# Performance work log

Hardware: AMD Instinct MI355X
Metric: run time of the kernel (lower is better)

## Reference

```python
import jax, jax.numpy as jnp
import numpy as np

B, L, C = 32, 8192, 64
LEVELS = 3  # detail kernels 3,5,9 with pads 1,2,4


def _conv1d(x, w, b, pad):
    # x: [B, C, L], w: [O, I, K] (torch Conv1d layout), b: [O]
    y = jax.lax.conv_general_dilated(
        x, w, window_strides=(1,), padding=[(pad, pad)],
        dimension_numbers=('NCH', 'OIH', 'NCH'))
    return y + b[None, :, None]


def _block(xc, w1, b1, w2, b2, pad):
    # Conv1d(k) -> ReLU -> Conv1d(k=1)
    h = jax.nn.relu(_conv1d(xc, w1, b1, pad))
    return _conv1d(h, w2, b2, 0)


def setup_inputs() -> dict:
    key = jax.random.key(0)
    ks = jax.random.split(key, 20)
    s = 0.05  # keep activations stable
    inp = {
        'x': jax.random.normal(ks[0], (B, L, C), jnp.float32),
        'rec_weights': jnp.ones((LEVELS + 1,), jnp.float32) / (LEVELS + 1),
        'trend_w1': jax.random.normal(ks[1], (C, C, 3), jnp.float32) * s,
        'trend_b1': jnp.zeros((C,), jnp.float32),
        'trend_w2': jax.random.normal(ks[2], (C, C, 1), jnp.float32) * s,
        'trend_b2': jnp.zeros((C,), jnp.float32),
    }
    kernels = [3, 5, 9]
    for i, k in enumerate(kernels, start=1):
        inp[f'd{i}_w1'] = jax.random.normal(ks[2 + 2 * i], (C, C, k), jnp.float32) * s
        inp[f'd{i}_b1'] = jnp.zeros((C,), jnp.float32)
        inp[f'd{i}_w2'] = jax.random.normal(ks[3 + 2 * i], (C, C, 1), jnp.float32) * s
        inp[f'd{i}_b2'] = jnp.zeros((C,), jnp.float32)
    return inp


def reference(x, rec_weights,
              trend_w1, trend_b1, trend_w2, trend_b2,
              d1_w1, d1_b1, d1_w2, d1_b2,
              d2_w1, d2_b1, d2_w2, d2_b2,
              d3_w1, d3_b1, d3_w2, d3_b2):
    # component_fusion forward: x [B, L, C] -> [B, L, C]
    xc = jnp.transpose(x, (0, 2, 1))  # [B, C, L]
    trend = _block(xc, trend_w1, trend_b1, trend_w2, trend_b2, 1)
    d1 = _block(xc, d1_w1, d1_b1, d1_w2, d1_b2, 1)   # k=3, pad=1
    d2 = _block(xc, d2_w1, d2_b1, d2_w2, d2_b2, 2)   # k=5, pad=2
    d3 = _block(xc, d3_w1, d3_b1, d3_w2, d3_b2, 4)   # k=9, pad=4
    w = jax.nn.softmax(rec_weights)
    fused = w[0] * trend + w[1] * d1 + w[2] * d2 + w[3] * d3
    return jnp.transpose(fused, (0, 2, 1))
```

## Files before the change

### kernel.cpp

```cpp
#include <hip/hip_runtime.h>


constexpr int Bn = 32, Ln = 8192;
constexpr int NT = 256;
constexpr int HALO = 4;
constexpr int XROWS = NT + 2 * HALO;
constexpr int RS = 72;
constexpr int NSLICE = 24;

using bf16x8 = __attribute__((ext_vector_type(8))) __bf16;
using f32x4  = __attribute__((ext_vector_type(4))) float;
using u16x8  = __attribute__((ext_vector_type(8))) unsigned short;
using u16x4  = __attribute__((ext_vector_type(4))) unsigned short;
using s16x4  = __attribute__((ext_vector_type(4))) short;

struct Ptrs {
    const float* x;
    const float* rw;
    const float* w1[4];
    const float* b1[4];
    const float* w2[4];
    const float* b2[4];
};

__device__ __forceinline__ unsigned short f2bf(float f) {
    __bf16 h = (__bf16)f;
    return __builtin_bit_cast(unsigned short, h);
}

#if defined(__has_builtin)
#  if __has_builtin(__builtin_amdgcn_mfma_f32_16x16x16bf16_1k)
#    define HAVE_MFMA16 1
#  endif
#endif

__device__ __forceinline__ void mfma16(f32x4& c, u16x4 a, u16x4 b) {
#ifdef HAVE_MFMA16
    c = __builtin_amdgcn_mfma_f32_16x16x16bf16_1k(
            __builtin_bit_cast(s16x4, a), __builtin_bit_cast(s16x4, b), c, 0, 0, 0);
#else
    asm("v_mfma_f32_16x16x16_bf16 %0, %1, %2, %0" : "+v"(c) : "v"(a), "v"(b));
#endif
}

__device__ __forceinline__ void stage_slice(const unsigned short* __restrict__ frag,
                                            unsigned short* wbuf, int s, int tid) {
    const unsigned short* g = frag + (size_t)s * 4096 + tid * 8;
    unsigned short* l = wbuf + (s & 1) * 4096 + tid * 8;
    __builtin_amdgcn_global_load_lds(
        (const __attribute__((address_space(1))) unsigned int*)g,
        (__attribute__((address_space(3))) unsigned int*)l, 16, 0, 0);
    __builtin_amdgcn_global_load_lds(
        (const __attribute__((address_space(1))) unsigned int*)(g + 2048),
        (__attribute__((address_space(3))) unsigned int*)(l + 2048), 16, 0, 0);
}

__device__ __forceinline__ void wait_bar_vm2() {
    asm volatile("s_waitcnt vmcnt(2)" ::: "memory");
    __builtin_amdgcn_sched_barrier(0);
    __builtin_amdgcn_s_barrier();
    __builtin_amdgcn_sched_barrier(0);
}
__device__ __forceinline__ void wait_bar_vm0() {
    asm volatile("s_waitcnt vmcnt(0)" ::: "memory");
    __builtin_amdgcn_sched_barrier(0);
    __builtin_amdgcn_s_barrier();
    __builtin_amdgcn_sched_barrier(0);
}
__device__ __forceinline__ void end_bar() {
    __builtin_amdgcn_sched_barrier(0);
    __builtin_amdgcn_s_barrier();
    __builtin_amdgcn_sched_barrier(0);
}

__global__ void prep_kernel(Ptrs p, unsigned short* __restrict__ frag, float* __restrict__ hdr) {
    int tid = threadIdx.x;
    float v0 = p.rw[0], v1 = p.rw[1], v2 = p.rw[2], v3 = p.rw[3];
    float m = fmaxf(fmaxf(v0, v1), fmaxf(v2, v3));
    float e0 = expf(v0 - m), e1 = expf(v1 - m), e2 = expf(v2 - m), e3 = expf(v3 - m);
    float s = e0 + e1 + e2 + e3;
    float w[4] = {e0 / s, e1 / s, e2 / s, e3 / s};

    if (blockIdx.x == 0) {
        if (tid < 4) hdr[tid] = w[tid];
        if (tid < 64) {
            float fb = 0.f;
            #pragma unroll
            for (int i = 0; i < 4; i++) fb += w[i] * p.b2[i][tid];
            hdr[4 + tid] = fb;
        }
    }

    const int kk[4] = {3, 3, 5, 9};
    const int sbase[4] = {0, 4, 8, 14};

    for (int idx = blockIdx.x * blockDim.x + tid; idx < NSLICE * 4096; idx += gridDim.x * blockDim.x) {
        int sl = idx >> 12;
        int e = idx & 4095;
        int br = 3;
        #pragma unroll
        for (int i = 2; i >= 0; i--) if (sl < sbase[i + 1]) br = i;
        int local = sl - sbase[br];
        unsigned short val;
        if (local < kk[br]) {
            int blk = e >> 9;
            int ks = blk >> 2, mt = blk & 3;
            int sub = e & 511;
            int lane = sub >> 3, j = sub & 7;
            int co = mt * 16 + (lane & 15);
            int ci = ks * 32 + (lane >> 4) * 8 + j;
            val = f2bf(p.w1[br][(co * 64 + ci) * kk[br] + local]);
        } else {
            int fi = e >> 8;
            int kb = fi >> 2, mt = fi & 3;
            int sub = e & 255;
            int lane = sub >> 2, j = sub & 3;
            int co = mt * 16 + (lane & 15);
            int ci = kb * 16 + (lane >> 4) * 4 + j;
            val = f2bf(w[br] * p.w2[br][co * 64 + ci]);
        }
        frag[idx] = val;
    }
}

template <int KK, int PP, int S0>
__device__ __forceinline__ void do_branch(const unsigned short* __restrict__ frag,
                                          unsigned short* wbuf,
                                          const float* b1l,
                                          const unsigned short* xs,
                                          int tid, int lane, int wl0,
                                          f32x4 (&fused)[4][4]) {
    int col = lane & 15, kg = lane >> 4;

    f32x4 acc[4][4];
    #pragma unroll
    for (int mt = 0; mt < 4; mt++)
        #pragma unroll
        for (int nt = 0; nt < 4; nt++)
            acc[mt][nt] = f32x4{0.f, 0.f, 0.f, 0.f};

    #pragma unroll
    for (int dk = 0; dk < KK; dk++) {
        stage_slice(frag, wbuf, S0 + dk + 1, tid);
        wait_bar_vm2();
        const unsigned short* wb = wbuf + ((S0 + dk) & 1) * 4096;
        #pragma unroll
        for (int ks = 0; ks < 2; ks++) {
            bf16x8 bfr[4];
            #pragma unroll
            for (int nt = 0; nt < 4; nt++) {
                int row = wl0 + nt * 16 + col + (HALO - PP) + dk;
                bfr[nt] = __builtin_bit_cast(bf16x8, *(const u16x8*)&xs[row * RS + ks * 32 + kg * 8]);
            }
            #pragma unroll
            for (int mt = 0; mt < 4; mt++) {
                bf16x8 afr = __builtin_bit_cast(bf16x8,
                    *(const u16x8*)(wb + (ks * 4 + mt) * 512 + lane * 8));
                #pragma unroll
                for (int nt = 0; nt < 4; nt++)
                    acc[mt][nt] = __builtin_amdgcn_mfma_f32_16x16x32_bf16(afr, bfr[nt], acc[mt][nt], 0, 0, 0);
            }
        }
        end_bar();
    }

    constexpr int SF2 = S0 + KK;
    constexpr bool HN = (SF2 + 1 < NSLICE);
    if constexpr (HN) stage_slice(frag, wbuf, SF2 + 1, tid);

    f32x4 bv[4];
    #pragma unroll
    for (int mt = 0; mt < 4; mt++) bv[mt] = *(const f32x4*)&b1l[mt * 16 + kg * 4];

    if constexpr (HN) wait_bar_vm2(); else wait_bar_vm0();
    const unsigned short* wb2 = wbuf + (SF2 & 1) * 4096;

    #pragma unroll
    for (int kb = 0; kb < 4; kb++) {
        u16x4 hb[4];
        #pragma unroll
        for (int nt = 0; nt < 4; nt++) {
            u16x4 h;
            #pragma unroll
            for (int r = 0; r < 4; r++) h[r] = f2bf(fmaxf(acc[kb][nt][r] + bv[kb][r], 0.f));
            hb[nt] = h;
        }
        #pragma unroll
        for (int mt = 0; mt < 4; mt++) {
            u16x4 afr = *(const u16x4*)(wb2 + (kb * 4 + mt) * 256 + lane * 4);
            #pragma unroll
            for (int nt = 0; nt < 4; nt++)
                mfma16(fused[mt][nt], afr, hb[nt]);
        }
    }
    if constexpr (HN) end_bar();
}

__global__ __launch_bounds__(256, 2) void wavelet_main(Ptrs p,
                                                       const unsigned short* __restrict__ frag,
                                                       const float* __restrict__ hdr,
                                                       float* __restrict__ out) {
    __shared__ unsigned short xs[XROWS * RS];
    __shared__ unsigned short wbuf[2 * 4096];
    __shared__ float b1l[4 * 64];
    __shared__ float fbl[64];

    int tid = threadIdx.x;
    int b = blockIdx.x >> 5;
    int t0 = (blockIdx.x & 31) * NT;

    stage_slice(frag, wbuf, 0, tid);

    {
        int c0 = (tid & 7) * 8;
        int rbase = tid >> 3;
        #pragma unroll
        for (int it = 0; it < 9; it++) {
            int rr = it * 32 + rbase;
            if (rr < XROWS) {
                int l = t0 + rr - HALO;
                u16x8 v = {0, 0, 0, 0, 0, 0, 0, 0};
                if (l >= 0 && l < Ln) {
                    const float* src = &p.x[((size_t)b * Ln + l) * 64 + c0];
                    f32x4 a0 = *(const f32x4*)src;
                    f32x4 a1 = *(const f32x4*)(src + 4);
                    #pragma unroll
                    for (int r = 0; r < 4; r++) { v[r] = f2bf(a0[r]); v[4 + r] = f2bf(a1[r]); }
                }
                *(u16x8*)&xs[rr * RS + c0] = v;
            }
        }
    }
    b1l[tid] = p.b1[tid >> 6][tid & 63];
    if (tid < 64) fbl[tid] = hdr[4 + tid];

    __syncthreads();

    int lane = tid & 63;
    int wl0 = (tid >> 6) * 64;
    int kg = lane >> 4;

    f32x4 fused[4][4];
    #pragma unroll
    for (int mt = 0; mt < 4; mt++)
        #pragma unroll
        for (int nt = 0; nt < 4; nt++)
            fused[mt][nt] = f32x4{0.f, 0.f, 0.f, 0.f};

    do_branch<3, 1, 0 >(frag, wbuf, b1l + 0 * 64, xs, tid, lane, wl0, fused);
    do_branch<3, 1, 4 >(frag, wbuf, b1l + 1 * 64, xs, tid, lane, wl0, fused);
    do_branch<5, 2, 8 >(frag, wbuf, b1l + 2 * 64, xs, tid, lane, wl0, fused);
    do_branch<9, 4, 14>(frag, wbuf, b1l + 3 * 64, xs, tid, lane, wl0, fused);

#ifndef HAVE_MFMA16
    asm volatile("s_nop 7\ns_nop 7");
#endif

    int col = lane & 15;
    f32x4 fb[4];
    #pragma unroll
    for (int mt = 0; mt < 4; mt++) fb[mt] = *(const f32x4*)&fbl[mt * 16 + kg * 4];
    #pragma unroll
    for (int mt = 0; mt < 4; mt++) {
        #pragma unroll
        for (int nt = 0; nt < 4; nt++) {
            int l = t0 + wl0 + nt * 16 + col;
            f32x4 v;
            #pragma unroll
            for (int r = 0; r < 4; r++) v[r] = fused[mt][nt][r] + fb[mt][r];
            *(f32x4*)&out[((size_t)b * Ln + l) * 64 + mt * 16 + kg * 4] = v;
        }
    }
}

extern "C" void kernel_launch(void* const* d_in, const int* in_sizes, int n_in,
                              void* d_out, int out_size, void* d_ws, size_t ws_size,
                              hipStream_t stream) {
    Ptrs p;
    p.x  = (const float*)d_in[0];
    p.rw = (const float*)d_in[1];
    for (int i = 0; i < 4; i++) {
        p.w1[i] = (const float*)d_in[2 + 4 * i];
        p.b1[i] = (const float*)d_in[3 + 4 * i];
        p.w2[i] = (const float*)d_in[4 + 4 * i];
        p.b2[i] = (const float*)d_in[5 + 4 * i];
    }
    float* hdr = (float*)d_ws;
    unsigned short* frag = (unsigned short*)((char*)d_ws + 512);

    hipLaunchKernelGGL(prep_kernel, dim3(96), dim3(256), 0, stream, p, frag, hdr);
    hipLaunchKernelGGL(wavelet_main, dim3(Bn * (Ln / NT)), dim3(256), 0, stream, p, frag, hdr,
                       (float*)d_out);
}
```

Baseline: 75.07 us.

## Deepen weight-slice prefetch to a four-slot LDS ring with one barrier per slice

Replaces the double-buffered weight staging with a 4-deep LDS ring. Each slice now prefetches three slices ahead, and the vmcnt wait thresholds are matched to how many loads are still in flight. The trailing barrier per slice is gone, because a buffer is only overwritten after the next slice's barrier guarantees every wave is done with it. The cost is 16 KB more LDS per block, and the first weight loads are issued after the x tile load instead of before it.

```diff
diff --git a/kernel.cpp b/kernel.cpp
--- a/kernel.cpp
+++ b/kernel.cpp
@@ -46,7 +46,7 @@
 __device__ __forceinline__ void stage_slice(const unsigned short* __restrict__ frag,
                                             unsigned short* wbuf, int s, int tid) {
     const unsigned short* g = frag + (size_t)s * 4096 + tid * 8;
-    unsigned short* l = wbuf + (s & 1) * 4096 + tid * 8;
+    unsigned short* l = wbuf + (s & 3) * 4096 + tid * 8;
     __builtin_amdgcn_global_load_lds(
         (const __attribute__((address_space(1))) unsigned int*)g,
         (__attribute__((address_space(3))) unsigned int*)l, 16, 0, 0);
@@ -55,22 +55,20 @@
         (__attribute__((address_space(3))) unsigned int*)(l + 2048), 16, 0, 0);
 }
 
-__device__ __forceinline__ void wait_bar_vm2() {
-    asm volatile("s_waitcnt vmcnt(2)" ::: "memory");
+template <int N>
+__device__ __forceinline__ void wait_bar() {
+    if constexpr (N == 4)      asm volatile("s_waitcnt vmcnt(4)" ::: "memory");
+    else if constexpr (N == 2) asm volatile("s_waitcnt vmcnt(2)" ::: "memory");
+    else                       asm volatile("s_waitcnt vmcnt(0)" ::: "memory");
     __builtin_amdgcn_sched_barrier(0);
     __builtin_amdgcn_s_barrier();
     __builtin_amdgcn_sched_barrier(0);
 }
-__device__ __forceinline__ void wait_bar_vm0() {
-    asm volatile("s_waitcnt vmcnt(0)" ::: "memory");
-    __builtin_amdgcn_sched_barrier(0);
-    __builtin_amdgcn_s_barrier();
-    __builtin_amdgcn_sched_barrier(0);
-}
-__device__ __forceinline__ void end_bar() {
-    __builtin_amdgcn_sched_barrier(0);
-    __builtin_amdgcn_s_barrier();
-    __builtin_amdgcn_sched_barrier(0);
+
+__device__ __forceinline__ void wait_bar_for(int S) {
+    if (S <= 21)      wait_bar<4>();
+    else if (S == 22) wait_bar<2>();
+    else              wait_bar<0>();
 }
 
 __global__ void prep_kernel(Ptrs p, unsigned short* __restrict__ frag, float* __restrict__ hdr) {
@@ -141,9 +139,9 @@
 
     #pragma unroll
     for (int dk = 0; dk < KK; dk++) {
-        stage_slice(frag, wbuf, S0 + dk + 1, tid);
-        wait_bar_vm2();
-        const unsigned short* wb = wbuf + ((S0 + dk) & 1) * 4096;
+        const int S = S0 + dk;
+        wait_bar_for(S);
+        const unsigned short* wb = wbuf + (S & 3) * 4096;
         #pragma unroll
         for (int ks = 0; ks < 2; ks++) {
             bf16x8 bfr[4];
@@ -161,19 +159,16 @@
                     acc[mt][nt] = __builtin_amdgcn_mfma_f32_16x16x32_bf16(afr, bfr[nt], acc[mt][nt], 0, 0, 0);
             }
         }
-        end_bar();
+        if (S + 3 < NSLICE) stage_slice(frag, wbuf, S + 3, tid);
     }
 
     constexpr int SF2 = S0 + KK;
-    constexpr bool HN = (SF2 + 1 < NSLICE);
-    if constexpr (HN) stage_slice(frag, wbuf, SF2 + 1, tid);
-
     f32x4 bv[4];
     #pragma unroll
     for (int mt = 0; mt < 4; mt++) bv[mt] = *(const f32x4*)&b1l[mt * 16 + kg * 4];
 
-    if constexpr (HN) wait_bar_vm2(); else wait_bar_vm0();
-    const unsigned short* wb2 = wbuf + (SF2 & 1) * 4096;
+    wait_bar_for(SF2);
+    const unsigned short* wb2 = wbuf + (SF2 & 3) * 4096;
 
     #pragma unroll
     for (int kb = 0; kb < 4; kb++) {
@@ -193,7 +188,7 @@
                 mfma16(fused[mt][nt], afr, hb[nt]);
         }
     }
-    if constexpr (HN) end_bar();
+    if (SF2 + 3 < NSLICE) stage_slice(frag, wbuf, SF2 + 3, tid);
 }
 
 __global__ __launch_bounds__(256, 2) void wavelet_main(Ptrs p,
@@ -201,15 +196,13 @@
                                                        const float* __restrict__ hdr,
                                                        float* __restrict__ out) {
     __shared__ unsigned short xs[XROWS * RS];
-    __shared__ unsigned short wbuf[2 * 4096];
+    __shared__ unsigned short wbuf[4 * 4096];
     __shared__ float b1l[4 * 64];
     __shared__ float fbl[64];
 
     int tid = threadIdx.x;
     int b = blockIdx.x >> 5;
     int t0 = (blockIdx.x & 31) * NT;
-
-    stage_slice(frag, wbuf, 0, tid);
 
     {
         int c0 = (tid & 7) * 8;
@@ -233,8 +226,16 @@
     }
     b1l[tid] = p.b1[tid >> 6][tid & 63];
     if (tid < 64) fbl[tid] = hdr[4 + tid];
-
-    __syncthreads();
+    __builtin_amdgcn_sched_barrier(0);
+
+    stage_slice(frag, wbuf, 0, tid);
+    stage_slice(frag, wbuf, 1, tid);
+    stage_slice(frag, wbuf, 2, tid);
+
+    asm volatile("s_waitcnt lgkmcnt(0)" ::: "memory");
+    __builtin_amdgcn_sched_barrier(0);
+    __builtin_amdgcn_s_barrier();
+    __builtin_amdgcn_sched_barrier(0);
 
     int lane = tid & 63;
     int wl0 = (tid >> 6) * 64;
```

Result: faster. 69.40 us (-7.6%).
